# Kernel optimization log

Measured on AMD Instinct MI355X. Metric: run time of the kernel, lower is better.

Reference implementation:

```python
import jax, jax.numpy as jnp
import numpy as np

EMBED_DIM = 1024
NUM_HEADS = 16
HEAD_DIM = EMBED_DIM // NUM_HEADS
B, T = 2, 2048


def setup_inputs() -> dict:
    key = jax.random.key(0)
    ks = jax.random.split(key, 10)
    s_in = 1.0 / np.sqrt(EMBED_DIM)
    s_hd = 1.0 / np.sqrt(HEAD_DIM)
    return {
        "hidden_states": jax.random.normal(ks[0], (B, T, EMBED_DIM), jnp.float32),
        "attn_mask": jnp.zeros((T, T), jnp.float32),
        # per-head parameter stacks (nn.Linear: y = x @ W^T + b); store W pre-transposed
        "W_q": jax.random.uniform(ks[1], (NUM_HEADS, EMBED_DIM, HEAD_DIM), jnp.float32, -s_in, s_in),
        "b_q": jax.random.uniform(ks[2], (NUM_HEADS, HEAD_DIM), jnp.float32, -s_in, s_in),
        "W_k": jax.random.uniform(ks[3], (NUM_HEADS, EMBED_DIM, HEAD_DIM), jnp.float32, -s_in, s_in),
        "b_k": jax.random.uniform(ks[4], (NUM_HEADS, HEAD_DIM), jnp.float32, -s_in, s_in),
        "W_v": jax.random.uniform(ks[5], (NUM_HEADS, EMBED_DIM, HEAD_DIM), jnp.float32, -s_in, s_in),
        "b_v": jax.random.uniform(ks[6], (NUM_HEADS, HEAD_DIM), jnp.float32, -s_in, s_in),
        "W_o": jax.random.uniform(ks[7], (NUM_HEADS, HEAD_DIM, EMBED_DIM), jnp.float32, -s_hd, s_hd),
        "b_o": jax.random.uniform(ks[8], (NUM_HEADS, EMBED_DIM), jnp.float32, -s_hd, s_hd),
        "gate": jnp.ones((NUM_HEADS,), jnp.float32),
    }


def reference(hidden_states, attn_mask, W_q, b_q, W_k, b_k, W_v, b_v, W_o, b_o, gate):
    # All heads: state='active', consent=True (defaults); dropout in eval mode.
    scale = 1.0 / np.sqrt(HEAD_DIM)
    # Q,K,V: [B,H,T,hd]
    Q = jnp.einsum("btd,hde->bhte", hidden_states, W_q) + b_q[None, :, None, :]
    K = jnp.einsum("btd,hde->bhte", hidden_states, W_k) + b_k[None, :, None, :]
    V = jnp.einsum("btd,hde->bhte", hidden_states, W_v) + b_v[None, :, None, :]
    scores = jnp.einsum("bhte,bhse->bhts", Q, K) * scale + attn_mask[None, None, :, :]
    weights = jax.nn.softmax(scores, axis=-1)
    out = jnp.einsum("bhts,bhse->bhte", weights, V)  # [B,H,T,hd]
    # per-head scalar norm: mean over (B,T) of L2 norm along head_dim, floored at 1e-5
    denom = jnp.maximum(
        jnp.sqrt(jnp.sum(out * out, axis=-1)).mean(axis=(0, 2)), 1e-5
    )  # [H]
    out_n = out / denom[None, :, None, None]
    g = jnp.clip(gate, 0.0, 1.0)  # gate_factor = 1.0 for 'active' heads
    # projected per head: (out_n @ W_o + b_o) * g; then sum over heads / H
    proj = (jnp.einsum("bhte,hed->bhtd", out_n, W_o) + b_o[None, :, None, :]) * g[None, :, None, None]
    return proj.sum(axis=1) / NUM_HEADS
```

## Files before the change

### kernel.cpp

```cpp
#include <hip/hip_runtime.h>
#include <hip/hip_bf16.h>
#include <math.h>

#define EMBED_DIM 1024
#define NUM_HEADS 16
#define HEAD_DIM  64
#define B_SZ      2
#define T_SZ      2048
#define BT        (B_SZ * T_SZ)
#define LOG2E     1.44269504088896340736f
#define QSCALE    (0.125f * LOG2E)
#define SOFT_OFF  8.0f

typedef short bf16x8 __attribute__((ext_vector_type(8)));
typedef float f32x4  __attribute__((ext_vector_type(4)));

#define MFMA16(a, b, c) __builtin_amdgcn_mfma_f32_16x16x32_bf16((a), (b), (c), 0, 0, 0)

__device__ inline short f2bf(float f) {
    unsigned u = __builtin_bit_cast(unsigned, f);
    u = (u + 0x7fffu + ((u >> 16) & 1u)) >> 16;
    return (short)u;
}
__device__ inline float bf2f(short s) {
    unsigned u = ((unsigned)(unsigned short)s) << 16;
    return __builtin_bit_cast(float, u);
}
__device__ inline unsigned pk2(float a, float b) {
#if __has_builtin(__builtin_amdgcn_cvt_pk_bf16_f32)
    typedef __bf16 bf2_t __attribute__((ext_vector_type(2)));
    bf2_t t = __builtin_amdgcn_cvt_pk_bf16_f32(a, b);
    return __builtin_bit_cast(unsigned, t);
#else
    return (unsigned)(unsigned short)f2bf(a) | ((unsigned)(unsigned short)f2bf(b) << 16);
#endif
}

__device__ inline void gld16(const short* g, short* lds) {
    __builtin_amdgcn_global_load_lds(
        (const __attribute__((address_space(1))) void*)g,
        (__attribute__((address_space(3))) void*)lds, 16, 0, 0);
}

__device__ inline bf16x8 frag_swz(const short* tile, int R, int C) {
    return *(const bf16x8*)(tile + R * 64 + ((C ^ (R & 7)) << 3));
}

__device__ inline float red_add64(float v) {
    v += __shfl_xor(v, 1); v += __shfl_xor(v, 2); v += __shfl_xor(v, 4);
    v += __shfl_xor(v, 8); v += __shfl_xor(v, 16); v += __shfl_xor(v, 32);
    return v;
}

__global__ __launch_bounds__(256) void cvt_in_kernel(
    const float* __restrict__ hs, short* __restrict__ hsb)
{
    const long i = ((long)blockIdx.x * 256 + threadIdx.x) * 4;
    const float4 v = *(const float4*)(hs + i);
    ushort4 o; o.x = f2bf(v.x); o.y = f2bf(v.y); o.z = f2bf(v.z); o.w = f2bf(v.w);
    *(ushort4*)(hsb + i) = o;
}

__global__ __launch_bounds__(256) void transpose_w_kernel(
    const float* __restrict__ Wq, const float* __restrict__ Wk,
    const float* __restrict__ Wv, const float* __restrict__ Wo,
    short* __restrict__ Wqt, short* __restrict__ Wkt,
    short* __restrict__ Wvt, short* __restrict__ WoT)
{
    const int arr = blockIdx.z, h = blockIdx.y;
    const float* src; short* dst; int R, C;
    if (arr == 0)      { src = Wq; dst = Wqt; R = 1024; C = 64; }
    else if (arr == 1) { src = Wk; dst = Wkt; R = 1024; C = 64; }
    else if (arr == 2) { src = Wv; dst = Wvt; R = 1024; C = 64; }
    else               { src = Wo; dst = WoT; R = 64;   C = 1024; }
    src += (long)h * 65536; dst += (long)h * 65536;

    const int ct = C / 32;
    const int tr = blockIdx.x / ct, tc = blockIdx.x % ct;
    __shared__ float tile[32][33];
    const int tx = threadIdx.x & 31, ty = threadIdx.x >> 5;
    #pragma unroll
    for (int i = 0; i < 4; ++i) {
        const int r = ty + 8 * i;
        tile[r][tx] = src[(long)(tr * 32 + r) * C + tc * 32 + tx];
    }
    __syncthreads();
    #pragma unroll
    for (int i = 0; i < 4; ++i) {
        const int r = ty + 8 * i;
        dst[(long)(tc * 32 + r) * R + tr * 32 + tx] = f2bf(tile[tx][r]);
    }
}

__global__ __launch_bounds__(256) void qkv_mfma_kernel(
    const short* __restrict__ hsb,
    const short* __restrict__ Wt,
    const float* __restrict__ bq, const float* __restrict__ bk,
    const float* __restrict__ bv,
    short* __restrict__ Qb, short* __restrict__ Kb, short* __restrict__ Vtb)
{
    const int m0 = blockIdx.x * 128;
    const int n0 = blockIdx.y * 128;
    __shared__ short As[128 * 64];
    __shared__ short Bs[128 * 64];

    const int tid = threadIdx.x, lane = tid & 63, w = tid >> 6;
    const int wm = w & 1, wn = w >> 1;
    const int quad = lane >> 4, l15 = lane & 15;

    f32x4 acc[4][4] = {};

    for (int k0 = 0; k0 < 1024; k0 += 64) {
        __syncthreads();
        #pragma unroll
        for (int t = 0; t < 4; ++t) {
            const int r0 = w * 32 + t * 8;
            const int r  = r0 + (lane >> 3);
            const int cg = (lane & 7) ^ (r & 7);
            gld16(hsb + (long)(m0 + r) * 1024 + k0 + cg * 8, &As[r0 * 64]);
            gld16(Wt  + (long)(n0 + r) * 1024 + k0 + cg * 8, &Bs[r0 * 64]);
        }
        __syncthreads();
        #pragma unroll
        for (int ks = 0; ks < 2; ++ks) {
            bf16x8 af[4];
            #pragma unroll
            for (int ms = 0; ms < 4; ++ms)
                af[ms] = frag_swz(As, wm * 64 + ms * 16 + l15, ks * 4 + quad);
            #pragma unroll
            for (int ns = 0; ns < 4; ++ns) {
                const bf16x8 bfr = frag_swz(Bs, wn * 64 + ns * 16 + l15, ks * 4 + quad);
                #pragma unroll
                for (int ms = 0; ms < 4; ++ms)
                    acc[ms][ns] = MFMA16(af[ms], bfr, acc[ms][ns]);
            }
        }
    }

    #pragma unroll
    for (int ns = 0; ns < 4; ++ns) {
        const int n    = n0 + wn * 64 + ns * 16 + l15;
        const int type = n >> 10;
        const int h    = (n >> 6) & 15;
        const int e    = n & 63;
        const float bias = (type == 0 ? bq : type == 1 ? bk : bv)[h * 64 + e];
        #pragma unroll
        for (int ms = 0; ms < 4; ++ms) {
            const int mbase = m0 + wm * 64 + ms * 16 + quad * 4;
            const int bb = mbase >> 11, t0 = mbase & 2047;
            if (type == 2) {
                const int tp = (t0 & ~63) | (t0 & 35) | ((t0 & 12) << 1) | ((t0 & 16) >> 2);
                ushort4 pk;
                pk.x = (unsigned short)f2bf(acc[ms][ns][0] + bias);
                pk.y = (unsigned short)f2bf(acc[ms][ns][1] + bias);
                pk.z = (unsigned short)f2bf(acc[ms][ns][2] + bias);
                pk.w = (unsigned short)f2bf(acc[ms][ns][3] + bias);
                *(ushort4*)&Vtb[((long)(bb * 16 + h) * 64 + e) * 2048 + tp] = pk;
            } else {
                #pragma unroll
                for (int r = 0; r < 4; ++r) {
                    const float v = acc[ms][ns][r] + bias;
                    const long off = ((long)(bb * 16 + h) * 2048 + (t0 + r)) * 64 + e;
                    if (type == 0) Qb[off] = f2bf(v * QSCALE);
                    else           Kb[off] = f2bf(v);
                }
            }
        }
    }
}

__global__ __launch_bounds__(256) void attn_mfma_kernel(
    const short* __restrict__ Qb, const short* __restrict__ Kb,
    const short* __restrict__ Vtb, const float* __restrict__ maskf,
    short* __restrict__ Ob, float* __restrict__ denomsum)
{
    const int q0 = blockIdx.x * 128;
    const int h  = blockIdx.y, b = blockIdx.z;
    const long bh = ((long)b * 16 + h) * (long)T_SZ * 64;

    __shared__ short Ks[64 * 64];
    __shared__ short Vs[64 * 64];
    __shared__ float wred[4];

    const int tid = threadIdx.x, lane = tid & 63, w = tid >> 6;
    const int quad = lane >> 4, l15 = lane & 15;
    const int qrowA = q0 + w * 32 + l15;

    const short* Kg = Kb + bh;
    const short* Vg = Vtb + bh;

    bf16x8 qf[2][2];
    #pragma unroll
    for (int qs = 0; qs < 2; ++qs)
        #pragma unroll
        for (int ks = 0; ks < 2; ++ks)
            qf[qs][ks] = *(const bf16x8*)(Qb + bh +
                (long)(qrowA + qs * 16) * 64 + ks * 32 + quad * 8);

    f32x4 o[2][4] = {};
    float lp[2] = {0.f, 0.f};

    const float* mrowA = maskf + (long)qrowA * 2048 + quad * 4;

    for (int kt = 0; kt < 32; ++kt) {
        const int kv0 = kt * 64;

        float4 mv[2][4];
        #pragma unroll
        for (int qs = 0; qs < 2; ++qs)
            #pragma unroll
            for (int kb = 0; kb < 4; ++kb)
                mv[qs][kb] = *(const float4*)(mrowA + (long)qs * 16 * 2048 + kv0 + kb * 16);

        __syncthreads();
        #pragma unroll
        for (int t = 0; t < 2; ++t) {
            const int r0 = w * 16 + t * 8;
            const int r  = r0 + (lane >> 3);
            const int cg = (lane & 7) ^ (r & 7);
            gld16(Kg + (long)(kv0 + r) * 64 + cg * 8, &Ks[r0 * 64]);
            gld16(Vg + (long)r * 2048 + kv0 + cg * 8, &Vs[r0 * 64]);
        }
        __syncthreads();

        #pragma unroll
        for (int qs = 0; qs < 2; ++qs) {
            f32x4 s[4];
            #pragma unroll
            for (int kb = 0; kb < 4; ++kb) {
                s[kb][0] = fmaf(mv[qs][kb].x, LOG2E, -SOFT_OFF);
                s[kb][1] = fmaf(mv[qs][kb].y, LOG2E, -SOFT_OFF);
                s[kb][2] = fmaf(mv[qs][kb].z, LOG2E, -SOFT_OFF);
                s[kb][3] = fmaf(mv[qs][kb].w, LOG2E, -SOFT_OFF);
            }
            #pragma unroll
            for (int ks = 0; ks < 2; ++ks)
                #pragma unroll
                for (int kb = 0; kb < 4; ++kb) {
                    const bf16x8 kf = frag_swz(Ks, kb * 16 + l15, ks * 4 + quad);
                    s[kb] = MFMA16(kf, qf[qs][ks], s[kb]);
                }

            float rs = 0.f;
            unsigned w0[4], w1[4];
            #pragma unroll
            for (int kb = 0; kb < 4; ++kb) {
                const float p0 = exp2f(s[kb][0]);
                const float p1 = exp2f(s[kb][1]);
                const float p2 = exp2f(s[kb][2]);
                const float p3 = exp2f(s[kb][3]);
                rs += (p0 + p1) + (p2 + p3);
                w0[kb] = pk2(p0, p1);
                w1[kb] = pk2(p2, p3);
            }
            lp[qs] += rs;

            #pragma unroll
            for (int kbp = 0; kbp < 2; ++kbp) {
                const uint4 u = {w0[2 * kbp], w1[2 * kbp], w0[2 * kbp + 1], w1[2 * kbp + 1]};
                const bf16x8 pb = __builtin_bit_cast(bf16x8, u);
                #pragma unroll
                for (int eb = 0; eb < 4; ++eb) {
                    const bf16x8 va = frag_swz(Vs, eb * 16 + l15, kbp * 4 + quad);
                    o[qs][eb] = MFMA16(va, pb, o[qs][eb]);
                }
            }
        }
    }

    float tot = 0.f;
    #pragma unroll
    for (int qs = 0; qs < 2; ++qs) {
        float lf = lp[qs];
        lf += __shfl_xor(lf, 16);
        lf += __shfl_xor(lf, 32);
        const float inv = 1.f / lf;
        float ss = 0.f;
        #pragma unroll
        for (int eb = 0; eb < 4; ++eb) {
            o[qs][eb] *= inv;
            #pragma unroll
            for (int r = 0; r < 4; ++r) ss += o[qs][eb][r] * o[qs][eb][r];
        }
        ss += __shfl_xor(ss, 16);
        ss += __shfl_xor(ss, 32);
        tot += sqrtf(ss);

        const int qrow = qrowA + qs * 16;
        #pragma unroll
        for (int eb = 0; eb < 4; ++eb) {
            uint2 pk;
            pk.x = pk2(o[qs][eb][0], o[qs][eb][1]);
            pk.y = pk2(o[qs][eb][2], o[qs][eb][3]);
            *(uint2*)&Ob[((long)(b * 2048 + qrow)) * 1024 + h * 64 + eb * 16 + quad * 4] = pk;
        }
    }
    const float wsum = red_add64(tot) * 0.25f;
    if (lane == 0) wred[w] = wsum;
    __syncthreads();
    if (tid == 0)
        atomicAdd(&denomsum[h], wred[0] + wred[1] + wred[2] + wred[3]);
}

__global__ __launch_bounds__(256) void scale_w_kernel(
    short* __restrict__ WoT, const float* __restrict__ denomsum,
    const float* __restrict__ gate)
{
    __shared__ float sh[16];
    if (threadIdx.x < 16) {
        const float g  = fminf(fmaxf(gate[threadIdx.x], 0.f), 1.f);
        const float dn = fmaxf(denomsum[threadIdx.x] * (1.f / (float)BT), 1e-5f);
        sh[threadIdx.x] = g / (dn * (float)NUM_HEADS);
    }
    __syncthreads();
    const long i = ((long)blockIdx.x * 256 + threadIdx.x) * 4;
    const float sc = sh[(int)(i >> 16)];
    ushort4 v = *(ushort4*)(WoT + i);
    v.x = (unsigned short)f2bf(bf2f((short)v.x) * sc);
    v.y = (unsigned short)f2bf(bf2f((short)v.y) * sc);
    v.z = (unsigned short)f2bf(bf2f((short)v.z) * sc);
    v.w = (unsigned short)f2bf(bf2f((short)v.w) * sc);
    *(ushort4*)(WoT + i) = v;
}

__global__ __launch_bounds__(256) void oproj_mfma_kernel(
    const short* __restrict__ Ob,
    const short* __restrict__ WoT,
    const float* __restrict__ bo,
    const float* __restrict__ gate,
    float* __restrict__ out)
{
    const int m0 = blockIdx.x * 128;
    const int n0 = blockIdx.y * 128;
    __shared__ short As[2][128 * 64];
    __shared__ short Bs[2][128 * 64];

    const int tid = threadIdx.x, lane = tid & 63, w = tid >> 6;
    const int wm = w & 1, wn = w >> 1;
    const int quad = lane >> 4, l15 = lane & 15;

    auto stage = [&](int h, int buf) {
        #pragma unroll
        for (int t = 0; t < 4; ++t) {
            const int r0 = w * 32 + t * 8;
            const int r  = r0 + (lane >> 3);
            const int cg = (lane & 7) ^ (r & 7);
            gld16(Ob + (long)(m0 + r) * 1024 + h * 64 + cg * 8, &As[buf][r0 * 64]);
            gld16(WoT + (long)h * 65536 + (long)(n0 + r) * 64 + cg * 8, &Bs[buf][r0 * 64]);
        }
    };

    f32x4 acc[4][4] = {};
    stage(0, 0);

    for (int h = 0; h < 16; ++h) {
        const int cur = h & 1;
        __syncthreads();
        if (h < 15) stage(h + 1, cur ^ 1);
        #pragma unroll
        for (int ks = 0; ks < 2; ++ks) {
            bf16x8 af[4];
            #pragma unroll
            for (int ms = 0; ms < 4; ++ms)
                af[ms] = frag_swz(&As[cur][0], wm * 64 + ms * 16 + l15, ks * 4 + quad);
            #pragma unroll
            for (int ns = 0; ns < 4; ++ns) {
                const bf16x8 bfr = frag_swz(&Bs[cur][0], wn * 64 + ns * 16 + l15, ks * 4 + quad);
                #pragma unroll
                for (int ms = 0; ms < 4; ++ms)
                    acc[ms][ns] = MFMA16(af[ms], bfr, acc[ms][ns]);
            }
        }
    }

    float gcl[16];
    #pragma unroll
    for (int hh = 0; hh < 16; ++hh)
        gcl[hh] = fminf(fmaxf(gate[hh], 0.f), 1.f) * (1.f / (float)NUM_HEADS);

    #pragma unroll
    for (int ns = 0; ns < 4; ++ns) {
        const int n = n0 + wn * 64 + ns * 16 + l15;
        float be = 0.f;
        #pragma unroll
        for (int hh = 0; hh < 16; ++hh) be += gcl[hh] * bo[hh * 1024 + n];
        #pragma unroll
        for (int ms = 0; ms < 4; ++ms) {
            const int m = m0 + wm * 64 + ms * 16 + quad * 4;
            #pragma unroll
            for (int r = 0; r < 4; ++r)
                out[(long)(m + r) * 1024 + n] = acc[ms][ns][r] + be;
        }
    }
}

extern "C" void kernel_launch(void* const* d_in, const int* in_sizes, int n_in,
                              void* d_out, int out_size, void* d_ws, size_t ws_size,
                              hipStream_t stream)
{
    const float* hs   = (const float*)d_in[0];
    const float* mask = (const float*)d_in[1];
    const float* Wq   = (const float*)d_in[2];
    const float* bq   = (const float*)d_in[3];
    const float* Wk   = (const float*)d_in[4];
    const float* bk   = (const float*)d_in[5];
    const float* Wv   = (const float*)d_in[6];
    const float* bv   = (const float*)d_in[7];
    const float* Wo   = (const float*)d_in[8];
    const float* bo   = (const float*)d_in[9];
    const float* gate = (const float*)d_in[10];
    float* out = (float*)d_out;

    char* ws = (char*)d_ws;
    const size_t MB = 1024 * 1024;
    short* hsb   = (short*)(ws);
    short* Wqt   = (short*)(ws + 8  * MB);
    short* Wkt   = (short*)(ws + 10 * MB);
    short* Wvt   = (short*)(ws + 12 * MB);
    short* WoT   = (short*)(ws + 14 * MB);
    short* Qb    = (short*)(ws + 16 * MB);
    short* Kb    = (short*)(ws + 24 * MB);
    short* Vtb   = (short*)(ws + 32 * MB);
    short* Ob    = (short*)(ws + 40 * MB);
    float* denomsum = (float*)(ws + 48 * MB);

    (void)hipMemsetAsync(denomsum, 0, NUM_HEADS * sizeof(float), stream);

    cvt_in_kernel<<<4096, 256, 0, stream>>>(hs, hsb);
    transpose_w_kernel<<<dim3(64, 16, 4), 256, 0, stream>>>(
        Wq, Wk, Wv, Wo, Wqt, Wkt, Wvt, WoT);
    qkv_mfma_kernel<<<dim3(32, 24), 256, 0, stream>>>(
        hsb, Wqt, bq, bk, bv, Qb, Kb, Vtb);
    attn_mfma_kernel<<<dim3(16, 16, 2), 256, 0, stream>>>(
        Qb, Kb, Vtb, mask, Ob, denomsum);
    scale_w_kernel<<<1024, 256, 0, stream>>>(WoT, denomsum, gate);
    oproj_mfma_kernel<<<dim3(32, 8), 256, 0, stream>>>(
        Ob, WoT, bo, gate, out);
}
```

Baseline: 262.1 us.

## Double-buffer K/V tiles in attention kernel and prefetch next mask tile

Splits the K/V shared-memory tiles into two buffers. The next tile's global-to-LDS loads are issued before computing on the current tile, with a manual vmcnt wait, and the next mask slice is prefetched after the QK MFMAs. K and V fragments are hoisted into registers before the MFMA batches, and s_setprio is raised around the MFMA bursts. The goal is to hide load latency behind compute, at the cost of twice the LDS and more register pressure, which may reduce occupancy. The hand-written vmcnt counts must match the number of outstanding loads or the results will be wrong.

```diff
diff --git a/kernel.cpp b/kernel.cpp
--- a/kernel.cpp
+++ b/kernel.cpp
@@ -178,8 +178,8 @@
     const int h  = blockIdx.y, b = blockIdx.z;
     const long bh = ((long)b * 16 + h) * (long)T_SZ * 64;
 
-    __shared__ short Ks[64 * 64];
-    __shared__ short Vs[64 * 64];
+    __shared__ short Ks[2][64 * 64];
+    __shared__ short Vs[2][64 * 64];
     __shared__ float wred[4];
 
     const int tid = threadIdx.x, lane = tid & 63, w = tid >> 6;
@@ -202,70 +202,112 @@
 
     const float* mrowA = maskf + (long)qrowA * 2048 + quad * 4;
 
-    for (int kt = 0; kt < 32; ++kt) {
+    auto stageKV = [&](int kt, int buf) {
         const int kv0 = kt * 64;
-
-        float4 mv[2][4];
-        #pragma unroll
-        for (int qs = 0; qs < 2; ++qs)
-            #pragma unroll
-            for (int kb = 0; kb < 4; ++kb)
-                mv[qs][kb] = *(const float4*)(mrowA + (long)qs * 16 * 2048 + kv0 + kb * 16);
-
-        __syncthreads();
         #pragma unroll
         for (int t = 0; t < 2; ++t) {
             const int r0 = w * 16 + t * 8;
             const int r  = r0 + (lane >> 3);
             const int cg = (lane & 7) ^ (r & 7);
-            gld16(Kg + (long)(kv0 + r) * 64 + cg * 8, &Ks[r0 * 64]);
-            gld16(Vg + (long)r * 2048 + kv0 + cg * 8, &Vs[r0 * 64]);
-        }
-        __syncthreads();
-
-        #pragma unroll
-        for (int qs = 0; qs < 2; ++qs) {
-            f32x4 s[4];
+            gld16(Kg + (long)(kv0 + r) * 64 + cg * 8, &Ks[buf][r0 * 64]);
+            gld16(Vg + (long)r * 2048 + kv0 + cg * 8, &Vs[buf][r0 * 64]);
+        }
+    };
+
+    float4 mv[2][4];
+    auto loadMask = [&](int kt) {
+        const int kv0 = kt * 64;
+        #pragma unroll
+        for (int qs = 0; qs < 2; ++qs)
+            #pragma unroll
+            for (int kb = 0; kb < 4; ++kb)
+                mv[qs][kb] = *(const float4*)(mrowA + (long)qs * 16 * 2048 + kv0 + kb * 16);
+    };
+
+    stageKV(0, 0);
+    loadMask(0);
+
+    for (int kt = 0; kt < 32; ++kt) {
+        const int cur = kt & 1;
+
+        __builtin_amdgcn_s_barrier();
+        asm volatile("" ::: "memory");
+        if (kt < 31) {
+            stageKV(kt + 1, cur ^ 1);
+            asm volatile("s_waitcnt vmcnt(4)" ::: "memory");
+        } else {
+            asm volatile("s_waitcnt vmcnt(0)" ::: "memory");
+        }
+        __builtin_amdgcn_s_barrier();
+        asm volatile("" ::: "memory");
+
+        f32x4 s[2][4];
+        #pragma unroll
+        for (int qs = 0; qs < 2; ++qs)
             #pragma unroll
             for (int kb = 0; kb < 4; ++kb) {
-                s[kb][0] = fmaf(mv[qs][kb].x, LOG2E, -SOFT_OFF);
-                s[kb][1] = fmaf(mv[qs][kb].y, LOG2E, -SOFT_OFF);
-                s[kb][2] = fmaf(mv[qs][kb].z, LOG2E, -SOFT_OFF);
-                s[kb][3] = fmaf(mv[qs][kb].w, LOG2E, -SOFT_OFF);
-            }
+                s[qs][kb][0] = fmaf(mv[qs][kb].x, LOG2E, -SOFT_OFF);
+                s[qs][kb][1] = fmaf(mv[qs][kb].y, LOG2E, -SOFT_OFF);
+                s[qs][kb][2] = fmaf(mv[qs][kb].z, LOG2E, -SOFT_OFF);
+                s[qs][kb][3] = fmaf(mv[qs][kb].w, LOG2E, -SOFT_OFF);
+            }
+
+        bf16x8 kf[2][4];
+        #pragma unroll
+        for (int ks = 0; ks < 2; ++ks)
+            #pragma unroll
+            for (int kb = 0; kb < 4; ++kb)
+                kf[ks][kb] = frag_swz(&Ks[cur][0], kb * 16 + l15, ks * 4 + quad);
+
+        __builtin_amdgcn_s_setprio(1);
+        #pragma unroll
+        for (int qs = 0; qs < 2; ++qs)
             #pragma unroll
             for (int ks = 0; ks < 2; ++ks)
                 #pragma unroll
-                for (int kb = 0; kb < 4; ++kb) {
-                    const bf16x8 kf = frag_swz(Ks, kb * 16 + l15, ks * 4 + quad);
-                    s[kb] = MFMA16(kf, qf[qs][ks], s[kb]);
-                }
-
+                for (int kb = 0; kb < 4; ++kb)
+                    s[qs][kb] = MFMA16(kf[ks][kb], qf[qs][ks], s[qs][kb]);
+        __builtin_amdgcn_s_setprio(0);
+
+        if (kt < 31) loadMask(kt + 1);
+
+        unsigned w0[2][4], w1[2][4];
+        #pragma unroll
+        for (int qs = 0; qs < 2; ++qs) {
             float rs = 0.f;
-            unsigned w0[4], w1[4];
             #pragma unroll
             for (int kb = 0; kb < 4; ++kb) {
-                const float p0 = exp2f(s[kb][0]);
-                const float p1 = exp2f(s[kb][1]);
-                const float p2 = exp2f(s[kb][2]);
-                const float p3 = exp2f(s[kb][3]);
+                const float p0 = exp2f(s[qs][kb][0]);
+                const float p1 = exp2f(s[qs][kb][1]);
+                const float p2 = exp2f(s[qs][kb][2]);
+                const float p3 = exp2f(s[qs][kb][3]);
                 rs += (p0 + p1) + (p2 + p3);
-                w0[kb] = pk2(p0, p1);
-                w1[kb] = pk2(p2, p3);
+                w0[qs][kb] = pk2(p0, p1);
+                w1[qs][kb] = pk2(p2, p3);
             }
             lp[qs] += rs;
-
+        }
+
+        bf16x8 va[2][4];
+        #pragma unroll
+        for (int kbp = 0; kbp < 2; ++kbp)
+            #pragma unroll
+            for (int eb = 0; eb < 4; ++eb)
+                va[kbp][eb] = frag_swz(&Vs[cur][0], eb * 16 + l15, kbp * 4 + quad);
+
+        __builtin_amdgcn_s_setprio(1);
+        #pragma unroll
+        for (int qs = 0; qs < 2; ++qs)
             #pragma unroll
             for (int kbp = 0; kbp < 2; ++kbp) {
-                const uint4 u = {w0[2 * kbp], w1[2 * kbp], w0[2 * kbp + 1], w1[2 * kbp + 1]};
+                const uint4 u = {w0[qs][2 * kbp], w1[qs][2 * kbp],
+                                 w0[qs][2 * kbp + 1], w1[qs][2 * kbp + 1]};
                 const bf16x8 pb = __builtin_bit_cast(bf16x8, u);
                 #pragma unroll
-                for (int eb = 0; eb < 4; ++eb) {
-                    const bf16x8 va = frag_swz(Vs, eb * 16 + l15, kbp * 4 + quad);
-                    o[qs][eb] = MFMA16(va, pb, o[qs][eb]);
-                }
-            }
-        }
+                for (int eb = 0; eb < 4; ++eb)
+                    o[qs][eb] = MFMA16(va[kbp][eb], pb, o[qs][eb]);
+            }
+        __builtin_amdgcn_s_setprio(0);
     }
 
     float tot = 0.f;
```

Result: no change. 262.5 us (+0.2%).

## Double-buffer K/V tiles in attention and use 8 waves of 16 query rows

Applied to the files above, without the earlier changes.

The attention kernel now uses 512 threads with each wave handling 16 query rows instead of 32. K/V tiles are double-buffered in LDS, with the next tile prefetched asynchronously and raw barriers plus explicit vmcnt waits replacing the __syncthreads pairs. The next mask tile is prefetched during compute, and exp2f is swapped for the hardware exp2 builtin. This aims to hide global-load latency and raise occupancy, at the cost of twice the LDS per block and less K/V reuse per wave.

```diff
diff --git a/kernel.cpp b/kernel.cpp
--- a/kernel.cpp
+++ b/kernel.cpp
@@ -33,6 +33,14 @@
     return __builtin_bit_cast(unsigned, t);
 #else
     return (unsigned)(unsigned short)f2bf(a) | ((unsigned)(unsigned short)f2bf(b) << 16);
+#endif
+}
+
+__device__ inline float ex2(float x) {
+#if __has_builtin(__builtin_amdgcn_exp2f)
+    return __builtin_amdgcn_exp2f(x);
+#else
+    return exp2f(x);
 #endif
 }
 
@@ -169,7 +177,7 @@
     }
 }
 
-__global__ __launch_bounds__(256) void attn_mfma_kernel(
+__global__ __launch_bounds__(512) void attn_mfma_kernel(
     const short* __restrict__ Qb, const short* __restrict__ Kb,
     const short* __restrict__ Vtb, const float* __restrict__ maskf,
     short* __restrict__ Ob, float* __restrict__ denomsum)
@@ -178,128 +186,138 @@
     const int h  = blockIdx.y, b = blockIdx.z;
     const long bh = ((long)b * 16 + h) * (long)T_SZ * 64;
 
-    __shared__ short Ks[64 * 64];
-    __shared__ short Vs[64 * 64];
-    __shared__ float wred[4];
+    __shared__ short Ks[2][64 * 64];
+    __shared__ short Vs[2][64 * 64];
+    __shared__ float wred[8];
 
     const int tid = threadIdx.x, lane = tid & 63, w = tid >> 6;
     const int quad = lane >> 4, l15 = lane & 15;
-    const int qrowA = q0 + w * 32 + l15;
+    const int qrow = q0 + w * 16 + l15;
 
     const short* Kg = Kb + bh;
     const short* Vg = Vtb + bh;
 
-    bf16x8 qf[2][2];
-    #pragma unroll
-    for (int qs = 0; qs < 2; ++qs)
+    bf16x8 qf[2];
+    #pragma unroll
+    for (int ks = 0; ks < 2; ++ks)
+        qf[ks] = *(const bf16x8*)(Qb + bh + (long)qrow * 64 + ks * 32 + quad * 8);
+
+    f32x4 o[4] = {};
+    float lp = 0.f;
+
+    const float* mrow = maskf + (long)qrow * 2048 + quad * 4;
+
+    auto stageKV = [&](int kt, int buf) {
+        const int kv0 = kt * 64;
+        const int r0 = w * 8;
+        const int r  = r0 + (lane >> 3);
+        const int cg = (lane & 7) ^ (r & 7);
+        gld16(Kg + (long)(kv0 + r) * 64 + cg * 8, &Ks[buf][r0 * 64]);
+        gld16(Vg + (long)r * 2048 + kv0 + cg * 8, &Vs[buf][r0 * 64]);
+    };
+
+    float4 mv[4];
+    auto loadMask = [&](int kt) {
+        const int kv0 = kt * 64;
+        #pragma unroll
+        for (int kb = 0; kb < 4; ++kb)
+            mv[kb] = *(const float4*)(mrow + kv0 + kb * 16);
+    };
+
+    stageKV(0, 0);
+    loadMask(0);
+
+    for (int kt = 0; kt < 32; ++kt) {
+        const int cur = kt & 1;
+
+        __builtin_amdgcn_s_barrier();
+        asm volatile("" ::: "memory");
+        if (kt < 31) {
+            stageKV(kt + 1, cur ^ 1);
+            asm volatile("s_waitcnt vmcnt(2)" ::: "memory");
+        } else {
+            asm volatile("s_waitcnt vmcnt(0)" ::: "memory");
+        }
+        __builtin_amdgcn_s_barrier();
+        asm volatile("" ::: "memory");
+
+        f32x4 s[4];
+        #pragma unroll
+        for (int kb = 0; kb < 4; ++kb) {
+            s[kb][0] = fmaf(mv[kb].x, LOG2E, -SOFT_OFF);
+            s[kb][1] = fmaf(mv[kb].y, LOG2E, -SOFT_OFF);
+            s[kb][2] = fmaf(mv[kb].z, LOG2E, -SOFT_OFF);
+            s[kb][3] = fmaf(mv[kb].w, LOG2E, -SOFT_OFF);
+        }
+
         #pragma unroll
         for (int ks = 0; ks < 2; ++ks)
-            qf[qs][ks] = *(const bf16x8*)(Qb + bh +
-                (long)(qrowA + qs * 16) * 64 + ks * 32 + quad * 8);
-
-    f32x4 o[2][4] = {};
-    float lp[2] = {0.f, 0.f};
-
-    const float* mrowA = maskf + (long)qrowA * 2048 + quad * 4;
-
-    for (int kt = 0; kt < 32; ++kt) {
-        const int kv0 = kt * 64;
-
-        float4 mv[2][4];
-        #pragma unroll
-        for (int qs = 0; qs < 2; ++qs)
-            #pragma unroll
-            for (int kb = 0; kb < 4; ++kb)
-                mv[qs][kb] = *(const float4*)(mrowA + (long)qs * 16 * 2048 + kv0 + kb * 16);
-
-        __syncthreads();
-        #pragma unroll
-        for (int t = 0; t < 2; ++t) {
-            const int r0 = w * 16 + t * 8;
-            const int r  = r0 + (lane >> 3);
-            const int cg = (lane & 7) ^ (r & 7);
-            gld16(Kg + (long)(kv0 + r) * 64 + cg * 8, &Ks[r0 * 64]);
-            gld16(Vg + (long)r * 2048 + kv0 + cg * 8, &Vs[r0 * 64]);
-        }
-        __syncthreads();
-
-        #pragma unroll
-        for (int qs = 0; qs < 2; ++qs) {
-            f32x4 s[4];
             #pragma unroll
             for (int kb = 0; kb < 4; ++kb) {
-                s[kb][0] = fmaf(mv[qs][kb].x, LOG2E, -SOFT_OFF);
-                s[kb][1] = fmaf(mv[qs][kb].y, LOG2E, -SOFT_OFF);
-                s[kb][2] = fmaf(mv[qs][kb].z, LOG2E, -SOFT_OFF);
-                s[kb][3] = fmaf(mv[qs][kb].w, LOG2E, -SOFT_OFF);
+                const bf16x8 kf = frag_swz(&Ks[cur][0], kb * 16 + l15, ks * 4 + quad);
+                s[kb] = MFMA16(kf, qf[ks], s[kb]);
             }
-            #pragma unroll
-            for (int ks = 0; ks < 2; ++ks)
-                #pragma unroll
-                for (int kb = 0; kb < 4; ++kb) {
-                    const bf16x8 kf = frag_swz(Ks, kb * 16 + l15, ks * 4 + quad);
-                    s[kb] = MFMA16(kf, qf[qs][ks], s[kb]);
-                }
-
-            float rs = 0.f;
-            unsigned w0[4], w1[4];
-            #pragma unroll
-            for (int kb = 0; kb < 4; ++kb) {
-                const float p0 = exp2f(s[kb][0]);
-                const float p1 = exp2f(s[kb][1]);
-                const float p2 = exp2f(s[kb][2]);
-                const float p3 = exp2f(s[kb][3]);
-                rs += (p0 + p1) + (p2 + p3);
-                w0[kb] = pk2(p0, p1);
-                w1[kb] = pk2(p2, p3);
+
+        if (kt < 31) loadMask(kt + 1);
+
+        float rs = 0.f;
+        unsigned w0[4], w1[4];
+        #pragma unroll
+        for (int kb = 0; kb < 4; ++kb) {
+            const float p0 = ex2(s[kb][0]);
+            const float p1 = ex2(s[kb][1]);
+            const float p2 = ex2(s[kb][2]);
+            const float p3 = ex2(s[kb][3]);
+            rs += (p0 + p1) + (p2 + p3);
+            w0[kb] = pk2(p0, p1);
+            w1[kb] = pk2(p2, p3);
+        }
+        lp += rs;
+
+        #pragma unroll
+        for (int kbp = 0; kbp < 2; ++kbp) {
+            const uint4 u = {w0[2 * kbp], w1[2 * kbp], w0[2 * kbp + 1], w1[2 * kbp + 1]};
+            const bf16x8 pb = __builtin_bit_cast(bf16x8, u);
+            #pragma unroll
+            for (int eb = 0; eb < 4; ++eb) {
+                const bf16x8 va = frag_swz(&Vs[cur][0], eb * 16 + l15, kbp * 4 + quad);
+                o[eb] = MFMA16(va, pb, o[eb]);
             }
-            lp[qs] += rs;
-
-            #pragma unroll
-            for (int kbp = 0; kbp < 2; ++kbp) {
-                const uint4 u = {w0[2 * kbp], w1[2 * kbp], w0[2 * kbp + 1], w1[2 * kbp + 1]};
-                const bf16x8 pb = __builtin_bit_cast(bf16x8, u);
-                #pragma unroll
-                for (int eb = 0; eb < 4; ++eb) {
-                    const bf16x8 va = frag_swz(Vs, eb * 16 + l15, kbp * 4 + quad);
-                    o[qs][eb] = MFMA16(va, pb, o[qs][eb]);
-                }
-            }
-        }
-    }
-
-    float tot = 0.f;
-    #pragma unroll
-    for (int qs = 0; qs < 2; ++qs) {
-        float lf = lp[qs];
-        lf += __shfl_xor(lf, 16);
-        lf += __shfl_xor(lf, 32);
-        const float inv = 1.f / lf;
-        float ss = 0.f;
-        #pragma unroll
-        for (int eb = 0; eb < 4; ++eb) {
-            o[qs][eb] *= inv;
-            #pragma unroll
-            for (int r = 0; r < 4; ++r) ss += o[qs][eb][r] * o[qs][eb][r];
-        }
-        ss += __shfl_xor(ss, 16);
-        ss += __shfl_xor(ss, 32);
-        tot += sqrtf(ss);
-
-        const int qrow = qrowA + qs * 16;
-        #pragma unroll
-        for (int eb = 0; eb < 4; ++eb) {
-            uint2 pk;
-            pk.x = pk2(o[qs][eb][0], o[qs][eb][1]);
-            pk.y = pk2(o[qs][eb][2], o[qs][eb][3]);
-            *(uint2*)&Ob[((long)(b * 2048 + qrow)) * 1024 + h * 64 + eb * 16 + quad * 4] = pk;
-        }
-    }
+        }
+    }
+
+    float lf = lp;
+    lf += __shfl_xor(lf, 16);
+    lf += __shfl_xor(lf, 32);
+    const float inv = 1.f / lf;
+    float ss = 0.f;
+    #pragma unroll
+    for (int eb = 0; eb < 4; ++eb) {
+        o[eb] *= inv;
+        #pragma unroll
+        for (int r = 0; r < 4; ++r) ss += o[eb][r] * o[eb][r];
+    }
+    ss += __shfl_xor(ss, 16);
+    ss += __shfl_xor(ss, 32);
+    const float tot = sqrtf(ss);
+
+    #pragma unroll
+    for (int eb = 0; eb < 4; ++eb) {
+        uint2 pk;
+        pk.x = pk2(o[eb][0], o[eb][1]);
+        pk.y = pk2(o[eb][2], o[eb][3]);
+        *(uint2*)&Ob[((long)(b * 2048 + qrow)) * 1024 + h * 64 + eb * 16 + quad * 4] = pk;
+    }
+
     const float wsum = red_add64(tot) * 0.25f;
     if (lane == 0) wred[w] = wsum;
     __syncthreads();
-    if (tid == 0)
-        atomicAdd(&denomsum[h], wred[0] + wred[1] + wred[2] + wred[3]);
+    if (tid == 0) {
+        float acc = 0.f;
+        #pragma unroll
+        for (int i = 0; i < 8; ++i) acc += wred[i];
+        atomicAdd(&denomsum[h], acc);
+    }
 }
 
 __global__ __launch_bounds__(256) void scale_w_kernel(
@@ -431,7 +449,7 @@
         Wq, Wk, Wv, Wo, Wqt, Wkt, Wvt, WoT);
     qkv_mfma_kernel<<<dim3(32, 24), 256, 0, stream>>>(
         hsb, Wqt, bq, bk, bv, Qb, Kb, Vtb);
-    attn_mfma_kernel<<<dim3(16, 16, 2), 256, 0, stream>>>(
+    attn_mfma_kernel<<<dim3(16, 16, 2), 512, 0, stream>>>(
         Qb, Kb, Vtb, mask, Ob, denomsum);
     scale_w_kernel<<<1024, 256, 0, stream>>>(WoT, denomsum, gate);
     oproj_mfma_kernel<<<dim3(32, 8), 256, 0, stream>>>(
```

Result: faster. 250.3 us (-4.5%).
